# Optimization experiments

Measured on AMD Instinct MI355X. Metric: run time of the kernel, lower is better.

## Reference

```python
import jax, jax.numpy as jnp
import numpy as np

NUM_HEADS = 16


def setup_inputs() -> dict:
    key = jax.random.key(0)
    ks = jax.random.split(key, 8)
    B, S, E = 2, 2048, 1024
    std = 0.02
    return {
        "q": jax.random.normal(ks[0], (B, S, E), dtype=jnp.float32),
        "k": jax.random.normal(ks[1], (B, S, E), dtype=jnp.float32),
        "v": jax.random.normal(ks[2], (B, S, E), dtype=jnp.float32),
        "Wq": jax.random.normal(ks[3], (E, E), dtype=jnp.float32) * std,
        "Wk": jax.random.normal(ks[4], (E, E), dtype=jnp.float32) * std,
        "Wv": jax.random.normal(ks[5], (E, E), dtype=jnp.float32) * std,
        "Wo": jax.random.normal(ks[6], (E, E), dtype=jnp.float32) * std,
        "bo": jnp.zeros((E,), dtype=jnp.float32),
    }


def reference(q, k, v, Wq, Wk, Wv, Wo, bo):
    B, S, E = q.shape
    H = NUM_HEADS
    D = E // H
    # projections (nn.Linear: x @ W.T)
    Q = (q @ Wq.T).reshape(B, S, H, D).transpose(0, 2, 1, 3)  # [B,H,S,D]
    K = (k @ Wk.T).reshape(B, S, H, D).transpose(0, 2, 1, 3)
    V = (v @ Wv.T).reshape(B, S, H, D).transpose(0, 2, 1, 3)
    scores = jnp.einsum("bhsd,bhtd->bhst", Q, K)  # [B,H,S,S]
    # causal mask applied before scaling (as in source; -inf/sqrt(d) == -inf)
    causal = jnp.tril(jnp.ones((S, S), dtype=bool))
    scores = jnp.where(causal, scores, -jnp.inf)
    scores = scores / np.sqrt(D).astype(np.float32)
    attn = jax.nn.softmax(scores, axis=-1)
    out = jnp.einsum("bhst,bhtd->bhsd", attn, V)  # [B,H,S,D]
    out = out.transpose(0, 2, 1, 3).reshape(B, S, E)
    return out @ Wo.T + bo
```

## Files before the change

kernel.cpp:

```cpp
#include <hip/hip_runtime.h>

typedef unsigned short u16;
typedef __bf16 bf16x8 __attribute__((ext_vector_type(8)));
typedef float f32x4 __attribute__((ext_vector_type(4)));
typedef unsigned u32x4 __attribute__((ext_vector_type(4)));

#define B_ 2
#define S_ 2048
#define E_ 1024
#define H_ 16
#define D_ 64
#define M_ (B_ * S_)

__device__ inline u16 f2bf(float f) {
  union { float f; unsigned int u; } c; c.f = f;
  unsigned int u = c.u;
  return (u16)((u + 0x7FFFu + ((u >> 16) & 1u)) >> 16);
}

__device__ inline f32x4 mfma16(bf16x8 a, bf16x8 b, f32x4 c) {
  return __builtin_amdgcn_mfma_f32_16x16x32_bf16(a, b, c, 0, 0, 0);
}

__device__ inline void gload16(const void* g, void* lds) {
  __builtin_amdgcn_global_load_lds(
      (const __attribute__((address_space(1))) unsigned int*)g,
      (__attribute__((address_space(3))) unsigned int*)lds, 16, 0, 0);
}

struct CvtArgs {
  const float* src[4];
  u16* dst[4];
  int n[4];
};

__global__ __launch_bounds__(256) void cvt_kernel(CvtArgs a) {
  const int arr = blockIdx.y;
  const int n = a.n[arr];
  const float* __restrict__ s = a.src[arr];
  u16* __restrict__ d = a.dst[arr];
  const int stride = gridDim.x * blockDim.x;
  for (int i = blockIdx.x * blockDim.x + threadIdx.x; i * 4 < n; i += stride) {
    const float4 f = *(const float4*)(s + 4 * i);
    ushort4 o;
    o.x = f2bf(f.x); o.y = f2bf(f.y); o.z = f2bf(f.z); o.w = f2bf(f.w);
    *(ushort4*)(d + 4 * i) = o;
  }
}

__global__ __launch_bounds__(256, 3) void qkv_gemm(
    const float* __restrict__ qf, const float* __restrict__ kf,
    const float* __restrict__ vf, const u16* __restrict__ Wqb,
    const u16* __restrict__ Wkb, const u16* __restrict__ Wvb,
    u16* __restrict__ Qh, u16* __restrict__ Kh, u16* __restrict__ Vt) {
  constexpr int BM = 128, BN = 128, BK = 32;
  __shared__ alignas(16) u16 As[3][BM * BK];
  __shared__ alignas(16) u16 Bs[3][BN * BK];

  const int wg = blockIdx.x;
  const int xcd = wg & 7, idx = wg >> 3;
  const int nb = idx & 7, mz = idx >> 3;
  const int z = mz >> 2;
  const int m0 = (xcd * 4 + (mz & 3)) * BM, n0 = nb * BN;

  const float* A = (z == 0) ? qf  : (z == 1) ? kf  : vf;
  const u16* Bt  = (z == 0) ? Wqb : (z == 1) ? Wkb : Wvb;
  u16* outp      = (z == 0) ? Qh  : (z == 1) ? Kh  : Vt;

  const int tid = threadIdx.x;
  const int wave = tid >> 6, lane = tid & 63;
  const int wm = (wave >> 1) * 64, wn = (wave & 1) * 64;
  const int fr = lane & 15, fc = lane >> 4;
  const int lrow = lane >> 2;
  const int lcol_sw = (((lane & 3) ^ ((lrow >> 1) & 3)) * 8);

  const int arow_sub = lane >> 3;
  const int acol = (lane & 7) * 4;
  const int a_chunkbase = wave * 2;

  f32x4 acc[4][4] = {};

  u16 *aA = As[0], *aB = As[1], *aC = As[2];
  u16 *bA = Bs[0], *bB = Bs[1], *bC = Bs[2];

  float4 areg0[4], areg1[4];

  auto loadA0 = [&](int k0) {
#pragma unroll
    for (int ci = 0; ci < 2; ++ci)
#pragma unroll
      for (int i2 = 0; i2 < 2; ++i2) {
        const int row = (a_chunkbase + ci) * 16 + i2 * 8 + arow_sub;
        areg0[ci * 2 + i2] = *(const float4*)(A + (size_t)(m0 + row) * E_ + k0 + acol);
      }
  };
  auto loadA1 = [&](int k0) {
#pragma unroll
    for (int ci = 0; ci < 2; ++ci)
#pragma unroll
      for (int i2 = 0; i2 < 2; ++i2) {
        const int row = (a_chunkbase + ci) * 16 + i2 * 8 + arow_sub;
        areg1[ci * 2 + i2] = *(const float4*)(A + (size_t)(m0 + row) * E_ + k0 + acol);
      }
  };
  auto writeA0 = [&](u16* as) {
#pragma unroll
    for (int ci = 0; ci < 2; ++ci)
#pragma unroll
      for (int i2 = 0; i2 < 2; ++i2) {
        const int rowLoc = i2 * 8 + arow_sub;
        const int row = (a_chunkbase + ci) * 16 + rowLoc;
        const float4 f = areg0[ci * 2 + i2];
        unsigned d0, d1;
        asm("v_cvt_pk_bf16_f32 %0, %1, %2" : "=v"(d0) : "v"(f.x), "v"(f.y));
        asm("v_cvt_pk_bf16_f32 %0, %1, %2" : "=v"(d1) : "v"(f.z), "v"(f.w));
        const int slot = (acol >> 3) ^ ((rowLoc >> 1) & 3);
        const int half = (acol >> 2) & 1;
        *(uint2*)(&as[row * 32 + slot * 8 + half * 4]) = make_uint2(d0, d1);
      }
  };
  auto writeA1 = [&](u16* as) {
#pragma unroll
    for (int ci = 0; ci < 2; ++ci)
#pragma unroll
      for (int i2 = 0; i2 < 2; ++i2) {
        const int rowLoc = i2 * 8 + arow_sub;
        const int row = (a_chunkbase + ci) * 16 + rowLoc;
        const float4 f = areg1[ci * 2 + i2];
        unsigned d0, d1;
        asm("v_cvt_pk_bf16_f32 %0, %1, %2" : "=v"(d0) : "v"(f.x), "v"(f.y));
        asm("v_cvt_pk_bf16_f32 %0, %1, %2" : "=v"(d1) : "v"(f.z), "v"(f.w));
        const int slot = (acol >> 3) ^ ((rowLoc >> 1) & 3);
        const int half = (acol >> 2) & 1;
        *(uint2*)(&as[row * 32 + slot * 8 + half * 4]) = make_uint2(d0, d1);
      }
  };
  auto loadB = [&](int k0, u16* bs) {
#pragma unroll
    for (int i = 0; i < 2; ++i) {
      const int chunk = wave * 2 + i;
      const int row = chunk * 16 + lrow;
      gload16(Bt + (size_t)(n0 + row) * E_ + k0 + lcol_sw, bs + chunk * 16 * BK);
    }
  };

  const int sl = (fc ^ ((fr >> 1) & 3)) * 8;

  auto compute = [&]() {
    bf16x8 af[4], bfr[4];
#pragma unroll
    for (int mi = 0; mi < 4; ++mi)
      af[mi] = *(const bf16x8*)&aA[(wm + mi * 16 + fr) * BK + sl];
#pragma unroll
    for (int ni = 0; ni < 4; ++ni)
      bfr[ni] = *(const bf16x8*)&bA[(wn + ni * 16 + fr) * BK + sl];
    __builtin_amdgcn_s_setprio(1);
#pragma unroll
    for (int mi = 0; mi < 4; ++mi)
#pragma unroll
      for (int ni = 0; ni < 4; ++ni)
        acc[mi][ni] = mfma16(af[mi], bfr[ni], acc[mi][ni]);
    __builtin_amdgcn_s_setprio(0);
    u16* tp;
    tp = aA; aA = aB; aB = aC; aC = tp;
    tp = bA; bA = bB; bB = bC; bC = tp;
  };

  constexpr int NK = E_ / BK;
  loadA0(0);
  asm volatile("s_waitcnt vmcnt(0)" ::: "memory");
  writeA0(aA);
  loadA1(1 * BK);  loadB(0, bA);
  loadA0(2 * BK);  loadB(1 * BK, bB);

  for (int tt = 0; tt < NK; tt += 2) {
    {
      const int t = tt;
      if (t + 3 < NK) {
        asm volatile("s_waitcnt vmcnt(6)" ::: "memory");
      } else {
        asm volatile("s_waitcnt vmcnt(0)" ::: "memory");
      }
      asm volatile("s_waitcnt lgkmcnt(0)" ::: "memory");
      __builtin_amdgcn_s_barrier();
      __builtin_amdgcn_sched_barrier(0);
      writeA1(aB);
      if (t + 3 < NK) loadA1((t + 3) * BK);
      if (t + 2 < NK) loadB((t + 2) * BK, bC);
      __builtin_amdgcn_sched_barrier(0);
      compute();
    }
    {
      const int t = tt + 1;
      if (t + 1 < NK) {
        if (t + 3 < NK) {
          asm volatile("s_waitcnt vmcnt(6)" ::: "memory");
        } else {
          asm volatile("s_waitcnt vmcnt(0)" ::: "memory");
        }
      } else {
        asm volatile("s_waitcnt vmcnt(0)" ::: "memory");
      }
      asm volatile("s_waitcnt lgkmcnt(0)" ::: "memory");
      __builtin_amdgcn_s_barrier();
      __builtin_amdgcn_sched_barrier(0);
      if (t + 1 < NK) writeA0(aB);
      if (t + 3 < NK) loadA0((t + 3) * BK);
      if (t + 2 < NK) loadB((t + 2) * BK, bC);
      __builtin_amdgcn_sched_barrier(0);
      compute();
    }
  }

#pragma unroll
  for (int mi = 0; mi < 4; ++mi)
#pragma unroll
    for (int ni = 0; ni < 4; ++ni)
#pragma unroll
      for (int r = 0; r < 4; ++r) {
        const int m = m0 + wm + mi * 16 + (fc << 2) + r;
        const int n = n0 + wn + ni * 16 + fr;
        const float v = acc[mi][ni][r];
        const int b = m >> 11, s = m & (S_ - 1), h = n >> 6, d = n & 63;
        if (z != 2) {
          outp[((((size_t)b * H_ + h) * S_ + s) << 6) + d] = f2bf(v);
        } else {
          outp[(((size_t)b * H_ + h) * D_ + d) * S_ + s] = f2bf(v);
        }
      }
}

__global__ __launch_bounds__(256, 4) void oproj_gemm(
    const u16* __restrict__ A, const u16* __restrict__ Bt,
    const float* __restrict__ bias, float* __restrict__ outp) {
  constexpr int BM = 64, BN = 128, BK = 32;
  __shared__ alignas(16) u16 As[3][BM * BK];
  __shared__ alignas(16) u16 Bs[3][BN * BK];

  const int wg = blockIdx.x;
  const int xcd = wg & 7, idx = wg >> 3;
  const int nb = idx & 7, mi_ = idx >> 3;
  const int m0 = (xcd * 8 + mi_) * BM, n0 = nb * BN;

  const int tid = threadIdx.x;
  const int wave = tid >> 6, lane = tid & 63;
  const int wm = (wave >> 1) * 32, wn = (wave & 1) * 64;
  const int fr = lane & 15, fc = lane >> 4;
  const int lrow = lane >> 2;
  const int lcol_sw = (((lane & 3) ^ ((lrow >> 1) & 3)) * 8);

  f32x4 acc[2][4] = {};

  u16 *aA = As[0], *aB = As[1], *aC = As[2];
  u16 *bA = Bs[0], *bB = Bs[1], *bC = Bs[2];

  auto stage = [&](int k0, u16* as, u16* bs) {
#pragma unroll
    for (int i = 0; i < 3; ++i) {
      const int c = wave + 4 * i;
      if (c < 4)
        gload16(A + (size_t)(m0 + c * 16 + lrow) * E_ + k0 + lcol_sw, as + c * 16 * BK);
      else
        gload16(Bt + (size_t)(n0 + (c - 4) * 16 + lrow) * E_ + k0 + lcol_sw,
                bs + (c - 4) * 16 * BK);
    }
  };

  constexpr int NK = E_ / BK;
  stage(0, aA, bA);
  stage(BK, aB, bB);

  const int sl = (fc ^ ((fr >> 1) & 3)) * 8;

  for (int t = 0; t < NK; ++t) {
    if (t + 1 < NK) {
      asm volatile("s_waitcnt vmcnt(3)" ::: "memory");
    } else {
      asm volatile("s_waitcnt vmcnt(0)" ::: "memory");
    }
    __builtin_amdgcn_s_barrier();
    __builtin_amdgcn_sched_barrier(0);

    if (t + 2 < NK) stage((t + 2) * BK, aC, bC);

    bf16x8 af[2], bfr[4];
#pragma unroll
    for (int mi = 0; mi < 2; ++mi)
      af[mi] = *(const bf16x8*)&aA[(wm + mi * 16 + fr) * BK + sl];
#pragma unroll
    for (int ni = 0; ni < 4; ++ni)
      bfr[ni] = *(const bf16x8*)&bA[(wn + ni * 16 + fr) * BK + sl];
    __builtin_amdgcn_s_setprio(1);
#pragma unroll
    for (int mi = 0; mi < 2; ++mi)
#pragma unroll
      for (int ni = 0; ni < 4; ++ni)
        acc[mi][ni] = mfma16(af[mi], bfr[ni], acc[mi][ni]);
    __builtin_amdgcn_s_setprio(0);

    u16* tp;
    tp = aA; aA = aB; aB = aC; aC = tp;
    tp = bA; bA = bB; bB = bC; bC = tp;
  }

#pragma unroll
  for (int mi = 0; mi < 2; ++mi)
#pragma unroll
    for (int ni = 0; ni < 4; ++ni)
#pragma unroll
      for (int r = 0; r < 4; ++r) {
        const int m = m0 + wm + mi * 16 + (fc << 2) + r;
        const int n = n0 + wn + ni * 16 + fr;
        outp[(size_t)m * E_ + n] = acc[mi][ni][r] + bias[n];
      }
}

__device__ __forceinline__ void stage_kv128(
    const u16* __restrict__ Kh_head, const u16* __restrict__ Vt_head,
    int kv0, u16* kb, u16* vb, int wq, int lane) {
#pragma unroll
  for (int hh = 0; hh < 2; ++hh)
    gload16(Kh_head + (size_t)(kv0 + hh * 64 + lane) * D_ + wq * 8,
            kb + wq * 1024 + hh * 512);
#pragma unroll
  for (int i = 0; i < 2; ++i) {
    const int c = 2 * wq + i;
    gload16(Vt_head + (size_t)lane * S_ + kv0 + c * 8, vb + c * 512);
  }
}

__global__ __launch_bounds__(512, 4) void flash_attn(
    const u16* __restrict__ Qh, const u16* __restrict__ Kh,
    const u16* __restrict__ Vt, u16* __restrict__ O) {
  __shared__ alignas(16) u16 Kb[2][8192];
  __shared__ alignas(16) u16 Vb[2][8192];

  const int i = blockIdx.x;
  const int ch = i >> 8, p = i & 255;
  const int j = (ch << 8) + ((ch & 1) ? (255 - p) : p);
  const int qt = 15 - (j >> 5);
  const int bh = j & 31;

  const int tid = threadIdx.x;
  const int wq = tid >> 6, lane = tid & 63;

  const int q0 = qt * 128;
  const int b = bh >> 4, h = bh & 15;
  constexpr float SC = 0.125f * 1.4426950408889634f;
  const int fr = lane & 15, fc = lane >> 4;

  const u16* Qbase = Qh + ((size_t)bh * S_ + q0 + wq * 16 + fr) * D_ + 8 * fc;
  const bf16x8 qf0 = *(const bf16x8*)Qbase;
  const bf16x8 qf1 = *(const bf16x8*)(Qbase + 32);
  const u16* Kh_head = Kh + (size_t)bh * S_ * D_;
  const u16* Vt_head = Vt + (size_t)bh * D_ * S_;

  float lacc = 0.f;
  f32x4 oacc[4] = {};
  const int nt = qt + 1;

  u16 *kA = Kb[0], *kB = Kb[1];
  u16 *vA = Vb[0], *vB = Vb[1];

  stage_kv128(Kh_head, Vt_head, 0, kA, vA, wq, lane);

  for (int t = 0; t < nt; ++t) {
    asm volatile("s_waitcnt vmcnt(0)" ::: "memory");
    __builtin_amdgcn_s_barrier();
    __builtin_amdgcn_sched_barrier(0);

    if (t + 1 < nt)
      stage_kv128(Kh_head, Vt_head, (t + 1) * 128, kB, vB, wq, lane);

    const u16* kb = kA;
    const u16* vb = vA;
    const bool diag = (t == nt - 1);
    const int qg = q0 + wq * 16 + fr;

#pragma unroll
    for (int hh = 0; hh < 2; ++hh) {
      const int kvb = t * 128 + hh * 64;

      f32x4 sacc[4] = {};
      __builtin_amdgcn_s_setprio(1);
#pragma unroll
      for (int ni = 0; ni < 4; ++ni) {
        const bf16x8 k0 = *(const bf16x8*)&kb[fc * 1024 + hh * 512 + (16 * ni + fr) * 8];
        const bf16x8 k1 = *(const bf16x8*)&kb[(fc + 4) * 1024 + hh * 512 + (16 * ni + fr) * 8];
        sacc[ni] = mfma16(k0, qf0, sacc[ni]);
        sacc[ni] = mfma16(k1, qf1, sacc[ni]);
      }
      __builtin_amdgcn_s_setprio(0);

#pragma unroll
      for (int ni = 0; ni < 4; ++ni)
#pragma unroll
        for (int r = 0; r < 4; ++r) {
          const int kvg = kvb + 16 * ni + 4 * fc + r;
          float pv;
          if (diag && kvg > qg) {
            pv = 0.f;
          } else {
            pv = __builtin_amdgcn_exp2f(sacc[ni][r] * SC);
          }
          sacc[ni][r] = pv;
          lacc += pv;
        }

      unsigned w[4][2];
#pragma unroll
      for (int ni = 0; ni < 4; ++ni) {
        asm("v_cvt_pk_bf16_f32 %0, %1, %2"
            : "=v"(w[ni][0]) : "v"(sacc[ni][0]), "v"(sacc[ni][1]));
        asm("v_cvt_pk_bf16_f32 %0, %1, %2"
            : "=v"(w[ni][1]) : "v"(sacc[ni][2]), "v"(sacc[ni][3]));
      }

      unsigned paw0[4], paw1[4];
#pragma unroll
      for (int pair = 0; pair < 2; ++pair) {
        unsigned xx[2], yy[2], tt2[2];
#pragma unroll
        for (int hh2 = 0; hh2 < 2; ++hh2) {
          unsigned a = w[2 * pair][hh2], bb = w[2 * pair + 1][hh2];
          asm volatile("v_permlane32_swap_b32 %0, %1" : "+v"(a), "+v"(bb));
          xx[hh2] = a; yy[hh2] = bb;
          const unsigned s = (fc & 1) ? a : bb;
          tt2[hh2] = (unsigned)__shfl_xor((int)s, 16);
        }
        unsigned* pw_ = pair ? paw1 : paw0;
        pw_[0] = (fc & 1) ? tt2[0] : xx[0];
        pw_[1] = (fc & 1) ? tt2[1] : xx[1];
        pw_[2] = (fc & 1) ? yy[0] : tt2[0];
        pw_[3] = (fc & 1) ? yy[1] : tt2[1];
      }
      bf16x8 pa0, pa1;
      {
        u32x4 t0 = {paw0[0], paw0[1], paw0[2], paw0[3]};
        u32x4 t1 = {paw1[0], paw1[1], paw1[2], paw1[3]};
        __builtin_memcpy(&pa0, &t0, 16);
        __builtin_memcpy(&pa1, &t1, 16);
      }

      __builtin_amdgcn_s_setprio(1);
#pragma unroll
      for (int nd = 0; nd < 4; ++nd) {
        const bf16x8 v0 = *(const bf16x8*)&vb[(hh * 8 + fc) * 512 + (16 * nd + fr) * 8];
        const bf16x8 v1 = *(const bf16x8*)&vb[(hh * 8 + fc + 4) * 512 + (16 * nd + fr) * 8];
        oacc[nd] = mfma16(pa0, v0, oacc[nd]);
        oacc[nd] = mfma16(pa1, v1, oacc[nd]);
      }
      __builtin_amdgcn_s_setprio(0);
    }

    u16* tk = kA; kA = kB; kB = tk;
    u16* tv = vA; vA = vB; vB = tv;
  }

  float l = lacc;
  l += __shfl_xor(l, 16);
  l += __shfl_xor(l, 32);
  float linv[4];
#pragma unroll
  for (int r = 0; r < 4; ++r)
    linv[r] = __builtin_amdgcn_rcpf(__shfl(l, 4 * fc + r));

#pragma unroll
  for (int nd = 0; nd < 4; ++nd) {
#pragma unroll
    for (int r = 0; r < 4; ++r) {
      const int qr = q0 + wq * 16 + (fc << 2) + r;
      const int d = 16 * nd + fr;
      const float v = oacc[nd][r] * linv[r];
      O[((size_t)b * S_ + qr) * E_ + h * D_ + d] = f2bf(v);
    }
  }
}

extern "C" void kernel_launch(void* const* d_in, const int* in_sizes, int n_in,
                              void* d_out, int out_size, void* d_ws, size_t ws_size,
                              hipStream_t stream) {
  const float* q  = (const float*)d_in[0];
  const float* k  = (const float*)d_in[1];
  const float* v  = (const float*)d_in[2];
  const float* Wq = (const float*)d_in[3];
  const float* Wk = (const float*)d_in[4];
  const float* Wv = (const float*)d_in[5];
  const float* Wo = (const float*)d_in[6];
  const float* bo = (const float*)d_in[7];

  const size_t nBSE = (size_t)M_ * E_;
  const size_t nEE  = (size_t)E_ * E_;
  u16* Wqb = (u16*)d_ws;
  u16* Wkb = Wqb + nEE;
  u16* Wvb = Wkb + nEE;
  u16* Wob = Wvb + nEE;
  u16* Qh  = Wob + nEE;
  u16* Kh  = Qh + nBSE;
  u16* Vt  = Kh + nBSE;
  u16* Oa  = Vt + nBSE;

  CvtArgs ca;
  ca.src[0] = Wq; ca.dst[0] = Wqb; ca.n[0] = (int)nEE;
  ca.src[1] = Wk; ca.dst[1] = Wkb; ca.n[1] = (int)nEE;
  ca.src[2] = Wv; ca.dst[2] = Wvb; ca.n[2] = (int)nEE;
  ca.src[3] = Wo; ca.dst[3] = Wob; ca.n[3] = (int)nEE;
  cvt_kernel<<<dim3(256, 4), 256, 0, stream>>>(ca);

  qkv_gemm<<<dim3(768), 256, 0, stream>>>(
      q, k, v, Wqb, Wkb, Wvb, Qh, Kh, Vt);
  flash_attn<<<dim3(512), 512, 0, stream>>>(Qh, Kh, Vt, Oa);
  oproj_gemm<<<dim3(512), 256, 0, stream>>>(Oa, Wob, bo, (float*)d_out);
}
```

Before: 102.7 us.

## Restructure QKV GEMM pipeline to process two K-tiles per barrier

Replaces the three-stage rotating LDS pipeline in the QKV projection GEMM with a ping-pong scheme that stages two K-tiles per buffer set. This halves the number of barriers and waits per K-step. LDS use grows to four tile buffers and launch bounds drop from 3 to 2 blocks per CU, so occupancy falls. Each iteration now waits with vmcnt(0), which may expose more global-load latency than the old partial waits did.

```diff
diff --git a/kernel.cpp b/kernel.cpp
--- a/kernel.cpp
+++ b/kernel.cpp
@@ -48,14 +48,14 @@
   }
 }
 
-__global__ __launch_bounds__(256, 3) void qkv_gemm(
+__global__ __launch_bounds__(256, 2) void qkv_gemm(
     const float* __restrict__ qf, const float* __restrict__ kf,
     const float* __restrict__ vf, const u16* __restrict__ Wqb,
     const u16* __restrict__ Wkb, const u16* __restrict__ Wvb,
     u16* __restrict__ Qh, u16* __restrict__ Kh, u16* __restrict__ Vt) {
   constexpr int BM = 128, BN = 128, BK = 32;
-  __shared__ alignas(16) u16 As[3][BM * BK];
-  __shared__ alignas(16) u16 Bs[3][BN * BK];
+  __shared__ alignas(16) u16 As[4][BM * BK];
+  __shared__ alignas(16) u16 Bs[4][BN * BK];
 
   const int wg = blockIdx.x;
   const int xcd = wg & 7, idx = wg >> 3;
@@ -80,8 +80,8 @@
 
   f32x4 acc[4][4] = {};
 
-  u16 *aA = As[0], *aB = As[1], *aC = As[2];
-  u16 *bA = Bs[0], *bB = Bs[1], *bC = Bs[2];
+  u16 *aP0 = As[0], *aP1 = As[1], *aQ0 = As[2], *aQ1 = As[3];
+  u16 *bP0 = Bs[0], *bP1 = Bs[1], *bQ0 = Bs[2], *bQ1 = Bs[3];
 
   float4 areg0[4], areg1[4];
 
@@ -146,14 +146,14 @@
 
   const int sl = (fc ^ ((fr >> 1) & 3)) * 8;
 
-  auto compute = [&]() {
+  auto compute = [&](const u16* ca, const u16* cb) {
     bf16x8 af[4], bfr[4];
 #pragma unroll
     for (int mi = 0; mi < 4; ++mi)
-      af[mi] = *(const bf16x8*)&aA[(wm + mi * 16 + fr) * BK + sl];
+      af[mi] = *(const bf16x8*)&ca[(wm + mi * 16 + fr) * BK + sl];
 #pragma unroll
     for (int ni = 0; ni < 4; ++ni)
-      bfr[ni] = *(const bf16x8*)&bA[(wn + ni * 16 + fr) * BK + sl];
+      bfr[ni] = *(const bf16x8*)&cb[(wn + ni * 16 + fr) * BK + sl];
     __builtin_amdgcn_s_setprio(1);
 #pragma unroll
     for (int mi = 0; mi < 4; ++mi)
@@ -161,55 +161,46 @@
       for (int ni = 0; ni < 4; ++ni)
         acc[mi][ni] = mfma16(af[mi], bfr[ni], acc[mi][ni]);
     __builtin_amdgcn_s_setprio(0);
+  };
+
+  constexpr int NT = E_ / BK;
+  constexpr int NE = NT / 2;
+  loadA0(0 * BK);
+  loadA1(1 * BK);
+  asm volatile("s_waitcnt vmcnt(0)" ::: "memory");
+  writeA0(aP0);
+  writeA1(aP1);
+  loadA0(2 * BK);
+  loadA1(3 * BK);
+  loadB(0 * BK, bP0);
+  loadB(1 * BK, bP1);
+
+  for (int e = 0; e < NE; ++e) {
+    asm volatile("s_waitcnt vmcnt(0)" ::: "memory");
+    asm volatile("s_waitcnt lgkmcnt(0)" ::: "memory");
+    __builtin_amdgcn_s_barrier();
+    __builtin_amdgcn_sched_barrier(0);
+
+    if (e + 1 < NE) {
+      writeA0(aQ0);
+      writeA1(aQ1);
+      if (e + 2 < NE) {
+        loadA0((2 * e + 4) * BK);
+        loadA1((2 * e + 5) * BK);
+      }
+      loadB((2 * e + 2) * BK, bQ0);
+      loadB((2 * e + 3) * BK, bQ1);
+    }
+    __builtin_amdgcn_sched_barrier(0);
+
+    compute(aP0, bP0);
+    compute(aP1, bP1);
+
     u16* tp;
-    tp = aA; aA = aB; aB = aC; aC = tp;
-    tp = bA; bA = bB; bB = bC; bC = tp;
-  };
-
-  constexpr int NK = E_ / BK;
-  loadA0(0);
-  asm volatile("s_waitcnt vmcnt(0)" ::: "memory");
-  writeA0(aA);
-  loadA1(1 * BK);  loadB(0, bA);
-  loadA0(2 * BK);  loadB(1 * BK, bB);
-
-  for (int tt = 0; tt < NK; tt += 2) {
-    {
-      const int t = tt;
-      if (t + 3 < NK) {
-        asm volatile("s_waitcnt vmcnt(6)" ::: "memory");
-      } else {
-        asm volatile("s_waitcnt vmcnt(0)" ::: "memory");
-      }
-      asm volatile("s_waitcnt lgkmcnt(0)" ::: "memory");
-      __builtin_amdgcn_s_barrier();
-      __builtin_amdgcn_sched_barrier(0);
-      writeA1(aB);
-      if (t + 3 < NK) loadA1((t + 3) * BK);
-      if (t + 2 < NK) loadB((t + 2) * BK, bC);
-      __builtin_amdgcn_sched_barrier(0);
-      compute();
-    }
-    {
-      const int t = tt + 1;
-      if (t + 1 < NK) {
-        if (t + 3 < NK) {
-          asm volatile("s_waitcnt vmcnt(6)" ::: "memory");
-        } else {
-          asm volatile("s_waitcnt vmcnt(0)" ::: "memory");
-        }
-      } else {
-        asm volatile("s_waitcnt vmcnt(0)" ::: "memory");
-      }
-      asm volatile("s_waitcnt lgkmcnt(0)" ::: "memory");
-      __builtin_amdgcn_s_barrier();
-      __builtin_amdgcn_sched_barrier(0);
-      if (t + 1 < NK) writeA0(aB);
-      if (t + 3 < NK) loadA0((t + 3) * BK);
-      if (t + 2 < NK) loadB((t + 2) * BK, bC);
-      __builtin_amdgcn_sched_barrier(0);
-      compute();
-    }
+    tp = aP0; aP0 = aQ0; aQ0 = tp;
+    tp = aP1; aP1 = aQ1; aQ1 = tp;
+    tp = bP0; bP0 = bQ0; bQ0 = tp;
+    tp = bP1; bP1 = bQ1; bQ1 = tp;
   }
 
 #pragma unroll
```

Measured after the change: 105.8 us. 1.03x slower.
